# Kernel tuning notes

Measured on AMD Instinct MI355X. Metric: run time of the kernel, lower is better.

## Reference

```python
import jax, jax.numpy as jnp
import numpy as np

N_LEVELS = 16
F_PER_LEVEL = 2
LOG2_HASH = 19
HASH_SIZE = 1 << LOG2_HASH
HASH_MASK = HASH_SIZE - 1
BASE_RES = 16
FINEST_RES = 512
N_POINTS = 1_000_000

_growth = np.exp((np.log(FINEST_RES) - np.log(BASE_RES)) / (N_LEVELS - 1))
RESOLUTIONS = [int(BASE_RES * _growth ** l) for l in range(N_LEVELS)]
# corner offsets in the torch loop order: dz outer, dy middle, dx inner
OFFSETS = np.array([[dx, dy, dz] for dz in (0, 1) for dy in (0, 1) for dx in (0, 1)], dtype=np.uint32)  # [8,3]
PRIMES = np.array([1, 2654435761, 805459861], dtype=np.uint32)


def setup_inputs() -> dict:
    key = jax.random.key(0)
    k1, k2 = jax.random.split(key)
    x = jax.random.normal(k1, (N_POINTS, 3), dtype=jnp.float32)
    # matches nn.init.uniform_(tbl.weight, -1e-4, 1e-4)
    tables = jax.random.uniform(k2, (N_LEVELS, HASH_SIZE, F_PER_LEVEL), minval=-1e-4, maxval=1e-4, dtype=jnp.float32)
    return {"x": x, "tables": tables}


def _encode_level(x_scaled, resolution, table):
    # x_scaled: [N,3] in [0,1]; table: [HASH_SIZE, F]
    xg = x_scaled * resolution
    xfloor = jnp.floor(xg)
    frac = xg - xfloor                                   # [N,3]
    offs = jnp.asarray(OFFSETS)                          # [8,3] uint32
    corners = xfloor.astype(jnp.uint32)[:, None, :] + offs[None]  # [N,8,3]
    primes = jnp.asarray(PRIMES)
    # spatial hash: XOR of coord*prime, mod 2^19 (power of two -> low-bit mask; uint32 wraparound is exact here)
    h = (corners[..., 0] * primes[0]) ^ (corners[..., 1] * primes[1]) ^ (corners[..., 2] * primes[2])
    idx = (h & jnp.uint32(HASH_MASK)).astype(jnp.int32)  # [N,8]
    feats = table[idx]                                   # [N,8,F]
    off_f = offs.astype(x_scaled.dtype)                  # [8,3]
    # trilinear weights: prod over dims of (frac if offset==1 else 1-frac)
    w = jnp.prod(off_f[None] * frac[:, None, :] + (1.0 - off_f[None]) * (1.0 - frac[:, None, :]), axis=-1)  # [N,8]
    return jnp.sum(w[..., None] * feats, axis=1)         # [N,F]


def reference(x, tables):
    x_min = x.min(axis=0, keepdims=True)
    x_max = x.max(axis=0, keepdims=True)
    x_scaled = (x - x_min) / (x_max - x_min + 1e-8)
    outs = [_encode_level(x_scaled, float(RESOLUTIONS[l]), tables[l]) for l in range(N_LEVELS)]
    return jnp.concatenate(outs, axis=-1)                # [N, 32]
```

## Files before the change

### kernel.cpp

```cpp
#include <hip/hip_runtime.h>
#include <cmath>

constexpr unsigned HASH_SIZE = 1u << 19;
constexpr unsigned HASH_MASK = HASH_SIZE - 1u;
constexpr unsigned P2 = 2654435761u;
constexpr unsigned P3 = 805459861u;
constexpr int NKEYS = 65536;
constexpr int NSHARD = 8;

struct ResArr { float r[16]; };
typedef float f4 __attribute__((ext_vector_type(4)));

__global__ __launch_bounds__(256) void he_minmax1(const float* __restrict__ x, int n,
                                                  float* __restrict__ part) {
    int tid = blockIdx.x * blockDim.x + threadIdx.x;
    int stride = gridDim.x * blockDim.x;
    float mn0 = INFINITY, mn1 = INFINITY, mn2 = INFINITY;
    float mx0 = -INFINITY, mx1 = -INFINITY, mx2 = -INFINITY;
    for (int i = tid; i < n; i += stride) {
        float a = x[3 * i + 0];
        float b = x[3 * i + 1];
        float c = x[3 * i + 2];
        mn0 = fminf(mn0, a); mx0 = fmaxf(mx0, a);
        mn1 = fminf(mn1, b); mx1 = fmaxf(mx1, b);
        mn2 = fminf(mn2, c); mx2 = fmaxf(mx2, c);
    }
    #pragma unroll
    for (int off = 32; off > 0; off >>= 1) {
        mn0 = fminf(mn0, __shfl_down(mn0, off));
        mn1 = fminf(mn1, __shfl_down(mn1, off));
        mn2 = fminf(mn2, __shfl_down(mn2, off));
        mx0 = fmaxf(mx0, __shfl_down(mx0, off));
        mx1 = fmaxf(mx1, __shfl_down(mx1, off));
        mx2 = fmaxf(mx2, __shfl_down(mx2, off));
    }
    __shared__ float s[6][4];
    int w = threadIdx.x >> 6;
    if ((threadIdx.x & 63) == 0) {
        s[0][w] = mn0; s[1][w] = mn1; s[2][w] = mn2;
        s[3][w] = mx0; s[4][w] = mx1; s[5][w] = mx2;
    }
    __syncthreads();
    if (threadIdx.x == 0) {
        float* p = part + 6 * blockIdx.x;
        p[0] = fminf(fminf(s[0][0], s[0][1]), fminf(s[0][2], s[0][3]));
        p[1] = fminf(fminf(s[1][0], s[1][1]), fminf(s[1][2], s[1][3]));
        p[2] = fminf(fminf(s[2][0], s[2][1]), fminf(s[2][2], s[2][3]));
        p[3] = fmaxf(fmaxf(s[3][0], s[3][1]), fmaxf(s[3][2], s[3][3]));
        p[4] = fmaxf(fmaxf(s[4][0], s[4][1]), fmaxf(s[4][2], s[4][3]));
        p[5] = fmaxf(fmaxf(s[5][0], s[5][1]), fmaxf(s[5][2], s[5][3]));
    }
}

__global__ __launch_bounds__(256) void he_minmax2(const float* __restrict__ part,
                                                  float* __restrict__ mm) {
    int t = threadIdx.x;
    const float* p = part + 6 * t;
    float mn0 = p[0], mn1 = p[1], mn2 = p[2];
    float mx0 = p[3], mx1 = p[4], mx2 = p[5];
    #pragma unroll
    for (int off = 32; off > 0; off >>= 1) {
        mn0 = fminf(mn0, __shfl_down(mn0, off));
        mn1 = fminf(mn1, __shfl_down(mn1, off));
        mn2 = fminf(mn2, __shfl_down(mn2, off));
        mx0 = fmaxf(mx0, __shfl_down(mx0, off));
        mx1 = fmaxf(mx1, __shfl_down(mx1, off));
        mx2 = fmaxf(mx2, __shfl_down(mx2, off));
    }
    __shared__ float s[6][4];
    int w = t >> 6;
    if ((t & 63) == 0) {
        s[0][w] = mn0; s[1][w] = mn1; s[2][w] = mn2;
        s[3][w] = mx0; s[4][w] = mx1; s[5][w] = mx2;
    }
    __syncthreads();
    if (t == 0) {
        mm[0] = fminf(fminf(s[0][0], s[0][1]), fminf(s[0][2], s[0][3]));
        mm[1] = fminf(fminf(s[1][0], s[1][1]), fminf(s[1][2], s[1][3]));
        mm[2] = fminf(fminf(s[2][0], s[2][1]), fminf(s[2][2], s[2][3]));
        mm[3] = fmaxf(fmaxf(s[3][0], s[3][1]), fmaxf(s[3][2], s[3][3]));
        mm[4] = fmaxf(fmaxf(s[4][0], s[4][1]), fmaxf(s[4][2], s[4][3]));
        mm[5] = fmaxf(fmaxf(s[5][0], s[5][1]), fmaxf(s[5][2], s[5][3]));
    }
}

__device__ __forceinline__ unsigned spread5(unsigned v) {
    return (v & 1u) | ((v & 2u) << 2) | ((v & 4u) << 4) | ((v & 8u) << 6) | ((v & 16u) << 8);
}

__global__ __launch_bounds__(256) void he_keys(const float* __restrict__ x, int n,
                                               const float* __restrict__ mm,
                                               unsigned* __restrict__ planes,
                                               unsigned short* __restrict__ keyA) {
    int i = blockIdx.x * 256 + threadIdx.x;
    if (i >= n) return;
    float den0 = (mm[3] - mm[0]) + 1e-8f;
    float den1 = (mm[4] - mm[1]) + 1e-8f;
    float den2 = (mm[5] - mm[2]) + 1e-8f;
    float xs = (x[3 * i + 0] - mm[0]) / den0;
    float ys = (x[3 * i + 1] - mm[1]) / den1;
    float zs = (x[3 * i + 2] - mm[2]) / den2;
    unsigned kx = min(63u, (unsigned)(xs * 64.0f));
    unsigned ky = min(31u, (unsigned)(ys * 32.0f));
    unsigned kz = min(31u, (unsigned)(zs * 32.0f));
    unsigned key = ((kx >> 5) << 15)
                 | (spread5(kx & 31u) << 2)
                 | (spread5(ky) << 1)
                 | spread5(kz);
    keyA[i] = (unsigned short)key;
    atomicAdd(&planes[(i & (NSHARD - 1)) * NKEYS + key], 1u);
}

__global__ __launch_bounds__(256) void he_scanShards(unsigned* __restrict__ planes,
                                                     unsigned* __restrict__ keytot) {
    int k = blockIdx.x * 256 + threadIdx.x;
    unsigned c[NSHARD];
    #pragma unroll
    for (int s = 0; s < NSHARD; ++s) c[s] = planes[s * NKEYS + k];
    unsigned run = 0;
    #pragma unroll
    for (int s = 0; s < NSHARD; ++s) {
        planes[s * NKEYS + k] = run;
        run += c[s];
    }
    keytot[k] = run;
}

__global__ __launch_bounds__(256) void he_scanA(unsigned* __restrict__ keytot,
                                                unsigned* __restrict__ bsum) {
    __shared__ unsigned s[256];
    int tid = threadIdx.x;
    int g = blockIdx.x * 256 + tid;
    unsigned v = keytot[g];
    s[tid] = v;
    __syncthreads();
    #pragma unroll
    for (int off = 1; off < 256; off <<= 1) {
        unsigned t = (tid >= off) ? s[tid - off] : 0u;
        __syncthreads();
        s[tid] += t;
        __syncthreads();
    }
    keytot[g] = s[tid] - v;
    if (tid == 255) bsum[blockIdx.x] = s[255];
}

__global__ __launch_bounds__(256) void he_scanB(unsigned* __restrict__ bsum) {
    __shared__ unsigned s[256];
    int tid = threadIdx.x;
    unsigned v = bsum[tid];
    s[tid] = v;
    __syncthreads();
    #pragma unroll
    for (int off = 1; off < 256; off <<= 1) {
        unsigned t = (tid >= off) ? s[tid - off] : 0u;
        __syncthreads();
        s[tid] += t;
        __syncthreads();
    }
    bsum[tid] = s[tid] - v;
}

__global__ __launch_bounds__(256) void he_scanC(unsigned* __restrict__ planes,
                                                const unsigned* __restrict__ keytot,
                                                const unsigned* __restrict__ bsum) {
    int g = blockIdx.x * 256 + threadIdx.x;
    unsigned base = keytot[g] + bsum[blockIdx.x];
    #pragma unroll
    for (int s = 0; s < NSHARD; ++s) planes[s * NKEYS + g] += base;
}

__global__ __launch_bounds__(256) void he_scatter(const unsigned short* __restrict__ keyA,
                                                  const float* __restrict__ x, int n,
                                                  const float* __restrict__ mm,
                                                  unsigned* __restrict__ planes,
                                                  f4* __restrict__ xsorted) {
    int i = blockIdx.x * 256 + threadIdx.x;
    if (i >= n) return;
    float den0 = (mm[3] - mm[0]) + 1e-8f;
    float den1 = (mm[4] - mm[1]) + 1e-8f;
    float den2 = (mm[5] - mm[2]) + 1e-8f;
    float xs = (x[3 * i + 0] - mm[0]) / den0;
    float ys = (x[3 * i + 1] - mm[1]) / den1;
    float zs = (x[3 * i + 2] - mm[2]) / den2;
    unsigned k = keyA[i];
    unsigned pos = atomicAdd(&planes[(i & (NSHARD - 1)) * NKEYS + k], 1u);
    f4 v;
    v.x = xs; v.y = ys; v.z = zs; v.w = __uint_as_float((unsigned)i);
    xsorted[pos] = v;
}

__device__ __forceinline__ void enc_core(float xs, float ys, float zs,
                                         const float* __restrict__ tables,
                                         const ResArr& res, float o[32]) {
    #pragma unroll
    for (int l = 0; l < 16; ++l) {
        float R = res.r[l];
        float xg = xs * R, yg = ys * R, zg = zs * R;
        float fx = floorf(xg), fy = floorf(yg), fz = floorf(zg);
        float tx = xg - fx, ty = yg - fy, tz = zg - fz;
        unsigned cx = (unsigned)fx, cy = (unsigned)fy, cz = (unsigned)fz;

        unsigned hx0 = cx,      hx1 = cx + 1u;
        unsigned hy0 = cy * P2, hy1 = hy0 + P2;
        unsigned hz0 = cz * P3, hz1 = hz0 + P3;

        const float2* __restrict__ T = (const float2*)tables + (size_t)l * HASH_SIZE;

        float2 f000 = T[(hx0 ^ hy0 ^ hz0) & HASH_MASK];
        float2 f100 = T[(hx1 ^ hy0 ^ hz0) & HASH_MASK];
        float2 f010 = T[(hx0 ^ hy1 ^ hz0) & HASH_MASK];
        float2 f110 = T[(hx1 ^ hy1 ^ hz0) & HASH_MASK];
        float2 f001 = T[(hx0 ^ hy0 ^ hz1) & HASH_MASK];
        float2 f101 = T[(hx1 ^ hy0 ^ hz1) & HASH_MASK];
        float2 f011 = T[(hx0 ^ hy1 ^ hz1) & HASH_MASK];
        float2 f111 = T[(hx1 ^ hy1 ^ hz1) & HASH_MASK];

        float wx0 = 1.0f - tx, wx1 = tx;
        float wy0 = 1.0f - ty, wy1 = ty;
        float wz0 = 1.0f - tz, wz1 = tz;

        float w000 = wx0 * wy0 * wz0;
        float w100 = wx1 * wy0 * wz0;
        float w010 = wx0 * wy1 * wz0;
        float w110 = wx1 * wy1 * wz0;
        float w001 = wx0 * wy0 * wz1;
        float w101 = wx1 * wy0 * wz1;
        float w011 = wx0 * wy1 * wz1;
        float w111 = wx1 * wy1 * wz1;

        float a0 = w000 * f000.x;
        float a1 = w000 * f000.y;
        a0 += w100 * f100.x;  a1 += w100 * f100.y;
        a0 += w010 * f010.x;  a1 += w010 * f010.y;
        a0 += w110 * f110.x;  a1 += w110 * f110.y;
        a0 += w001 * f001.x;  a1 += w001 * f001.y;
        a0 += w101 * f101.x;  a1 += w101 * f101.y;
        a0 += w011 * f011.x;  a1 += w011 * f011.y;
        a0 += w111 * f111.x;  a1 += w111 * f111.y;

        o[2 * l + 0] = a0;
        o[2 * l + 1] = a1;
    }
}

__device__ __forceinline__ int swz_block(int b, int nwg) {
    int q = nwg >> 3, r = nwg & 7;
    int xcd = b & 7, kk = b >> 3;
    return (xcd < r ? xcd * (q + 1) : r * (q + 1) + (xcd - r) * q) + kk;
}

__global__ __launch_bounds__(256) void he_encode_scatter(const f4* __restrict__ xsorted,
                                                         const float* __restrict__ tables,
                                                         float* __restrict__ out, int n, ResArr res) {
    int sb = swz_block(blockIdx.x, gridDim.x);
    int j = sb * 256 + threadIdx.x;
    if (j >= n) return;
    f4 p = xsorted[j];
    int i = (int)__float_as_uint(p.w);
    float o[32];
    enc_core(p.x, p.y, p.z, tables, res, o);
    float* op = out + (size_t)i * 32;
    #pragma unroll
    for (int k = 0; k < 8; ++k) {
        f4 v;
        v.x = o[4 * k + 0]; v.y = o[4 * k + 1]; v.z = o[4 * k + 2]; v.w = o[4 * k + 3];
        *(f4*)(op + 4 * k) = v;
    }
}

__global__ __launch_bounds__(256) void he_encode_plain(const float* __restrict__ x,
                                                       const float* __restrict__ tables,
                                                       const float* __restrict__ mm,
                                                       float* __restrict__ out, int n, ResArr res) {
    int i = blockIdx.x * 256 + threadIdx.x;
    if (i >= n) return;
    float den0 = (mm[3] - mm[0]) + 1e-8f;
    float den1 = (mm[4] - mm[1]) + 1e-8f;
    float den2 = (mm[5] - mm[2]) + 1e-8f;
    float xs = (x[3 * i + 0] - mm[0]) / den0;
    float ys = (x[3 * i + 1] - mm[1]) / den1;
    float zs = (x[3 * i + 2] - mm[2]) / den2;
    float o[32];
    enc_core(xs, ys, zs, tables, res, o);
    float* op = out + (size_t)i * 32;
    #pragma unroll
    for (int k = 0; k < 8; ++k) {
        f4 v;
        v.x = o[4 * k + 0]; v.y = o[4 * k + 1]; v.z = o[4 * k + 2]; v.w = o[4 * k + 3];
        __builtin_nontemporal_store(v, (f4*)(op + 4 * k));
    }
}

extern "C" void kernel_launch(void* const* d_in, const int* in_sizes, int n_in,
                              void* d_out, int out_size, void* d_ws, size_t ws_size,
                              hipStream_t stream) {
    const float* x = (const float*)d_in[0];
    const float* tables = (const float*)d_in[1];
    float* out = (float*)d_out;
    int n = in_sizes[0] / 3;

    char* w = (char*)d_ws;
    float*          mm      = (float*)w;
    float*          part    = (float*)(w + 4096);
    unsigned*       bsum    = (unsigned*)(w + 16384);
    unsigned*       keytot  = (unsigned*)(w + 32768);
    unsigned*       planes  = (unsigned*)(w + 524288);
    unsigned short* keyA    = (unsigned short*)(w + 0x300000);
    f4*             xsorted = (f4*)(w + 0x500000);

    const size_t NEED1 = 0x500000 + (size_t)16777216;
    int tier = (ws_size >= NEED1) ? 1 : 0;
    if (n > (1 << 20)) tier = 0;

    ResArr res;
    double growth = exp((log(512.0) - log(16.0)) / 15.0);
    for (int l = 0; l < 16; ++l) {
        res.r[l] = (float)(int)(16.0 * pow(growth, (double)l));
    }

    int blocks = (n + 255) / 256;

    he_minmax1<<<256, 256, 0, stream>>>(x, n, part);
    he_minmax2<<<1, 256, 0, stream>>>(part, mm);

    if (tier >= 1) {
        hipMemsetAsync(planes, 0, (size_t)NSHARD * NKEYS * 4, stream);
        he_keys<<<blocks, 256, 0, stream>>>(x, n, mm, planes, keyA);
        he_scanShards<<<NKEYS / 256, 256, 0, stream>>>(planes, keytot);
        he_scanA<<<NKEYS / 256, 256, 0, stream>>>(keytot, bsum);
        he_scanB<<<1, 256, 0, stream>>>(bsum);
        he_scanC<<<NKEYS / 256, 256, 0, stream>>>(planes, keytot, bsum);
        he_scatter<<<blocks, 256, 0, stream>>>(keyA, x, n, mm, planes, xsorted);
        he_encode_scatter<<<blocks, 256, 0, stream>>>(xsorted, tables, out, n, res);
    } else {
        he_encode_plain<<<blocks, 256, 0, stream>>>(x, tables, mm, out, n, res);
    }
}
```

Measured before the change: 328.1 us.

## Pair x-adjacent hash corners into 16-byte loads, fuse scan kernels, drop key buffer

```diff
diff --git a/kernel.cpp b/kernel.cpp
--- a/kernel.cpp
+++ b/kernel.cpp
@@ -88,10 +88,90 @@
     return (v & 1u) | ((v & 2u) << 2) | ((v & 4u) << 4) | ((v & 8u) << 6) | ((v & 16u) << 8);
 }
 
-__global__ __launch_bounds__(256) void he_keys(const float* __restrict__ x, int n,
+__device__ __forceinline__ unsigned morton_key(const float* __restrict__ x, int i,
+                                               const float* __restrict__ mm) {
+    float den0 = (mm[3] - mm[0]) + 1e-8f;
+    float den1 = (mm[4] - mm[1]) + 1e-8f;
+    float den2 = (mm[5] - mm[2]) + 1e-8f;
+    float xs = (x[3 * i + 0] - mm[0]) / den0;
+    float ys = (x[3 * i + 1] - mm[1]) / den1;
+    float zs = (x[3 * i + 2] - mm[2]) / den2;
+    unsigned kx = min(63u, (unsigned)(xs * 64.0f));
+    unsigned ky = min(31u, (unsigned)(ys * 32.0f));
+    unsigned kz = min(31u, (unsigned)(zs * 32.0f));
+    return ((kx >> 5) << 15)
+         | (spread5(kx & 31u) << 2)
+         | (spread5(ky) << 1)
+         | spread5(kz);
+}
+
+__global__ __launch_bounds__(256) void he_hist(const float* __restrict__ x, int n,
                                                const float* __restrict__ mm,
-                                               unsigned* __restrict__ planes,
-                                               unsigned short* __restrict__ keyA) {
+                                               unsigned* __restrict__ planes) {
+    int i = blockIdx.x * 256 + threadIdx.x;
+    if (i >= n) return;
+    unsigned key = morton_key(x, i, mm);
+    atomicAdd(&planes[(i & (NSHARD - 1)) * NKEYS + key], 1u);
+}
+
+__global__ __launch_bounds__(256) void he_scanSA(unsigned* __restrict__ planes,
+                                                 unsigned* __restrict__ keytot,
+                                                 unsigned* __restrict__ bsum) {
+    int tid = threadIdx.x;
+    int k = blockIdx.x * 256 + tid;
+    unsigned c[NSHARD];
+    #pragma unroll
+    for (int s = 0; s < NSHARD; ++s) c[s] = planes[s * NKEYS + k];
+    unsigned run = 0;
+    #pragma unroll
+    for (int s = 0; s < NSHARD; ++s) {
+        planes[s * NKEYS + k] = run;
+        run += c[s];
+    }
+    __shared__ unsigned sh[256];
+    unsigned v = run;
+    sh[tid] = v;
+    __syncthreads();
+    #pragma unroll
+    for (int off = 1; off < 256; off <<= 1) {
+        unsigned t = (tid >= off) ? sh[tid - off] : 0u;
+        __syncthreads();
+        sh[tid] += t;
+        __syncthreads();
+    }
+    keytot[k] = sh[tid] - v;
+    if (tid == 255) bsum[blockIdx.x] = sh[255];
+}
+
+__global__ __launch_bounds__(256) void he_scanB(unsigned* __restrict__ bsum) {
+    __shared__ unsigned s[256];
+    int tid = threadIdx.x;
+    unsigned v = bsum[tid];
+    s[tid] = v;
+    __syncthreads();
+    #pragma unroll
+    for (int off = 1; off < 256; off <<= 1) {
+        unsigned t = (tid >= off) ? s[tid - off] : 0u;
+        __syncthreads();
+        s[tid] += t;
+        __syncthreads();
+    }
+    bsum[tid] = s[tid] - v;
+}
+
+__global__ __launch_bounds__(256) void he_scanC(unsigned* __restrict__ planes,
+                                                const unsigned* __restrict__ keytot,
+                                                const unsigned* __restrict__ bsum) {
+    int g = blockIdx.x * 256 + threadIdx.x;
+    unsigned base = keytot[g] + bsum[blockIdx.x];
+    #pragma unroll
+    for (int s = 0; s < NSHARD; ++s) planes[s * NKEYS + g] += base;
+}
+
+__global__ __launch_bounds__(256) void he_scatter(const float* __restrict__ x, int n,
+                                                  const float* __restrict__ mm,
+                                                  unsigned* __restrict__ planes,
+                                                  f4* __restrict__ xsorted) {
     int i = blockIdx.x * 256 + threadIdx.x;
     if (i >= n) return;
     float den0 = (mm[3] - mm[0]) + 1e-8f;
@@ -107,84 +187,7 @@
                  | (spread5(kx & 31u) << 2)
                  | (spread5(ky) << 1)
                  | spread5(kz);
-    keyA[i] = (unsigned short)key;
-    atomicAdd(&planes[(i & (NSHARD - 1)) * NKEYS + key], 1u);
-}
-
-__global__ __launch_bounds__(256) void he_scanShards(unsigned* __restrict__ planes,
-                                                     unsigned* __restrict__ keytot) {
-    int k = blockIdx.x * 256 + threadIdx.x;
-    unsigned c[NSHARD];
-    #pragma unroll
-    for (int s = 0; s < NSHARD; ++s) c[s] = planes[s * NKEYS + k];
-    unsigned run = 0;
-    #pragma unroll
-    for (int s = 0; s < NSHARD; ++s) {
-        planes[s * NKEYS + k] = run;
-        run += c[s];
-    }
-    keytot[k] = run;
-}
-
-__global__ __launch_bounds__(256) void he_scanA(unsigned* __restrict__ keytot,
-                                                unsigned* __restrict__ bsum) {
-    __shared__ unsigned s[256];
-    int tid = threadIdx.x;
-    int g = blockIdx.x * 256 + tid;
-    unsigned v = keytot[g];
-    s[tid] = v;
-    __syncthreads();
-    #pragma unroll
-    for (int off = 1; off < 256; off <<= 1) {
-        unsigned t = (tid >= off) ? s[tid - off] : 0u;
-        __syncthreads();
-        s[tid] += t;
-        __syncthreads();
-    }
-    keytot[g] = s[tid] - v;
-    if (tid == 255) bsum[blockIdx.x] = s[255];
-}
-
-__global__ __launch_bounds__(256) void he_scanB(unsigned* __restrict__ bsum) {
-    __shared__ unsigned s[256];
-    int tid = threadIdx.x;
-    unsigned v = bsum[tid];
-    s[tid] = v;
-    __syncthreads();
-    #pragma unroll
-    for (int off = 1; off < 256; off <<= 1) {
-        unsigned t = (tid >= off) ? s[tid - off] : 0u;
-        __syncthreads();
-        s[tid] += t;
-        __syncthreads();
-    }
-    bsum[tid] = s[tid] - v;
-}
-
-__global__ __launch_bounds__(256) void he_scanC(unsigned* __restrict__ planes,
-                                                const unsigned* __restrict__ keytot,
-                                                const unsigned* __restrict__ bsum) {
-    int g = blockIdx.x * 256 + threadIdx.x;
-    unsigned base = keytot[g] + bsum[blockIdx.x];
-    #pragma unroll
-    for (int s = 0; s < NSHARD; ++s) planes[s * NKEYS + g] += base;
-}
-
-__global__ __launch_bounds__(256) void he_scatter(const unsigned short* __restrict__ keyA,
-                                                  const float* __restrict__ x, int n,
-                                                  const float* __restrict__ mm,
-                                                  unsigned* __restrict__ planes,
-                                                  f4* __restrict__ xsorted) {
-    int i = blockIdx.x * 256 + threadIdx.x;
-    if (i >= n) return;
-    float den0 = (mm[3] - mm[0]) + 1e-8f;
-    float den1 = (mm[4] - mm[1]) + 1e-8f;
-    float den2 = (mm[5] - mm[2]) + 1e-8f;
-    float xs = (x[3 * i + 0] - mm[0]) / den0;
-    float ys = (x[3 * i + 1] - mm[1]) / den1;
-    float zs = (x[3 * i + 2] - mm[2]) / den2;
-    unsigned k = keyA[i];
-    unsigned pos = atomicAdd(&planes[(i & (NSHARD - 1)) * NKEYS + k], 1u);
+    unsigned pos = atomicAdd(&planes[(i & (NSHARD - 1)) * NKEYS + key], 1u);
     f4 v;
     v.x = xs; v.y = ys; v.z = zs; v.w = __uint_as_float((unsigned)i);
     xsorted[pos] = v;
@@ -201,43 +204,48 @@
         float tx = xg - fx, ty = yg - fy, tz = zg - fz;
         unsigned cx = (unsigned)fx, cy = (unsigned)fy, cz = (unsigned)fz;
 
-        unsigned hx0 = cx,      hx1 = cx + 1u;
         unsigned hy0 = cy * P2, hy1 = hy0 + P2;
         unsigned hz0 = cz * P3, hz1 = hz0 + P3;
+        unsigned dx = cx ^ (cx + 1u);
+        bool odd = (cx & 1u) != 0u;
 
         const float2* __restrict__ T = (const float2*)tables + (size_t)l * HASH_SIZE;
-
-        float2 f000 = T[(hx0 ^ hy0 ^ hz0) & HASH_MASK];
-        float2 f100 = T[(hx1 ^ hy0 ^ hz0) & HASH_MASK];
-        float2 f010 = T[(hx0 ^ hy1 ^ hz0) & HASH_MASK];
-        float2 f110 = T[(hx1 ^ hy1 ^ hz0) & HASH_MASK];
-        float2 f001 = T[(hx0 ^ hy0 ^ hz1) & HASH_MASK];
-        float2 f101 = T[(hx1 ^ hy0 ^ hz1) & HASH_MASK];
-        float2 f011 = T[(hx0 ^ hy1 ^ hz1) & HASH_MASK];
-        float2 f111 = T[(hx1 ^ hy1 ^ hz1) & HASH_MASK];
 
         float wx0 = 1.0f - tx, wx1 = tx;
         float wy0 = 1.0f - ty, wy1 = ty;
         float wz0 = 1.0f - tz, wz1 = tz;
 
-        float w000 = wx0 * wy0 * wz0;
-        float w100 = wx1 * wy0 * wz0;
-        float w010 = wx0 * wy1 * wz0;
-        float w110 = wx1 * wy1 * wz0;
-        float w001 = wx0 * wy0 * wz1;
-        float w101 = wx1 * wy0 * wz1;
-        float w011 = wx0 * wy1 * wz1;
-        float w111 = wx1 * wy1 * wz1;
-
-        float a0 = w000 * f000.x;
-        float a1 = w000 * f000.y;
-        a0 += w100 * f100.x;  a1 += w100 * f100.y;
-        a0 += w010 * f010.x;  a1 += w010 * f010.y;
-        a0 += w110 * f110.x;  a1 += w110 * f110.y;
-        a0 += w001 * f001.x;  a1 += w001 * f001.y;
-        a0 += w101 * f101.x;  a1 += w101 * f101.y;
-        a0 += w011 * f011.x;  a1 += w011 * f011.y;
-        a0 += w111 * f111.x;  a1 += w111 * f111.y;
+        unsigned hyz0 = hy0 ^ hz0, hyz1 = hy1 ^ hz0, hyz2 = hy0 ^ hz1, hyz3 = hy1 ^ hz1;
+        float wyz0 = wy0 * wz0, wyz1 = wy1 * wz0, wyz2 = wy0 * wz1, wyz3 = wy1 * wz1;
+
+        float a0 = 0.0f, a1 = 0.0f;
+
+        #define CORNER_PAIR(HYZ, WYZ)                                         \
+        {                                                                     \
+            unsigned ia = (cx ^ (HYZ)) & HASH_MASK;                           \
+            f4 q = *(const f4*)(T + (ia & ~1u));                              \
+            bool hi = (ia & 1u) != 0u;                                        \
+            float fax = hi ? q.z : q.x;                                       \
+            float fay = hi ? q.w : q.y;                                       \
+            float fbx, fby;                                                   \
+            if (odd) {                                                        \
+                float2 fb = T[ia ^ dx];                                       \
+                fbx = fb.x; fby = fb.y;                                       \
+            } else {                                                          \
+                fbx = hi ? q.x : q.z;                                         \
+                fby = hi ? q.y : q.w;                                         \
+            }                                                                 \
+            float wA = wx0 * (WYZ);                                           \
+            float wB = wx1 * (WYZ);                                           \
+            a0 += wA * fax;  a1 += wA * fay;                                  \
+            a0 += wB * fbx;  a1 += wB * fby;                                  \
+        }
+
+        CORNER_PAIR(hyz0, wyz0);
+        CORNER_PAIR(hyz1, wyz1);
+        CORNER_PAIR(hyz2, wyz2);
+        CORNER_PAIR(hyz3, wyz3);
+        #undef CORNER_PAIR
 
         o[2 * l + 0] = a0;
         o[2 * l + 1] = a1;
@@ -288,7 +296,7 @@
     for (int k = 0; k < 8; ++k) {
         f4 v;
         v.x = o[4 * k + 0]; v.y = o[4 * k + 1]; v.z = o[4 * k + 2]; v.w = o[4 * k + 3];
-        __builtin_nontemporal_store(v, (f4*)(op + 4 * k));
+        *(f4*)(op + 4 * k) = v;
     }
 }
 
@@ -301,15 +309,14 @@
     int n = in_sizes[0] / 3;
 
     char* w = (char*)d_ws;
-    float*          mm      = (float*)w;
-    float*          part    = (float*)(w + 4096);
-    unsigned*       bsum    = (unsigned*)(w + 16384);
-    unsigned*       keytot  = (unsigned*)(w + 32768);
-    unsigned*       planes  = (unsigned*)(w + 524288);
-    unsigned short* keyA    = (unsigned short*)(w + 0x300000);
-    f4*             xsorted = (f4*)(w + 0x500000);
-
-    const size_t NEED1 = 0x500000 + (size_t)16777216;
+    float*    mm      = (float*)w;
+    float*    part    = (float*)(w + 4096);
+    unsigned* bsum    = (unsigned*)(w + 16384);
+    unsigned* keytot  = (unsigned*)(w + 32768);
+    unsigned* planes  = (unsigned*)(w + 524288);
+    f4*       xsorted = (f4*)(w + 0x300000);
+
+    const size_t NEED1 = 0x300000 + (size_t)16777216;
     int tier = (ws_size >= NEED1) ? 1 : 0;
     if (n > (1 << 20)) tier = 0;
 
@@ -326,12 +333,11 @@
 
     if (tier >= 1) {
         hipMemsetAsync(planes, 0, (size_t)NSHARD * NKEYS * 4, stream);
-        he_keys<<<blocks, 256, 0, stream>>>(x, n, mm, planes, keyA);
-        he_scanShards<<<NKEYS / 256, 256, 0, stream>>>(planes, keytot);
-        he_scanA<<<NKEYS / 256, 256, 0, stream>>>(keytot, bsum);
+        he_hist<<<blocks, 256, 0, stream>>>(x, n, mm, planes);
+        he_scanSA<<<NKEYS / 256, 256, 0, stream>>>(planes, keytot, bsum);
         he_scanB<<<1, 256, 0, stream>>>(bsum);
         he_scanC<<<NKEYS / 256, 256, 0, stream>>>(planes, keytot, bsum);
-        he_scatter<<<blocks, 256, 0, stream>>>(keyA, x, n, mm, planes, xsorted);
+        he_scatter<<<blocks, 256, 0, stream>>>(x, n, mm, planes, xsorted);
         he_encode_scatter<<<blocks, 256, 0, stream>>>(xsorted, tables, out, n, res);
     } else {
         he_encode_plain<<<blocks, 256, 0, stream>>>(x, tables, mm, out, n, res);
```

Result: slower. 445.1 us (+35.7%).
